# Kernel optimization log

Hardware: AMD Instinct MI355X
Metric: run time of the kernel (lower is better)

Reference implementation:

```python
import jax, jax.numpy as jnp
import numpy as np

N, G, H = 262144, 512, 16
EPS = 1e-5

Q_MAT = jnp.array([[0.0, 0.0, 1.0], [1.0, 0.0, 0.0], [0.0, 1.0, 0.0]], dtype=jnp.float32)
Q_TENSOR = jnp.kron(Q_MAT, Q_MAT)  # 9x9


def setup_inputs() -> dict:
    key = jax.random.key(0)
    ks = jax.random.split(key, 10)
    # sorted node->graph ids, every graph guaranteed non-empty
    gid = jnp.sort(jnp.concatenate([
        jnp.arange(G, dtype=jnp.int32),
        jax.random.randint(ks[0], (N - G,), 0, G, dtype=jnp.int32)]))
    return {
        'x00': jax.random.normal(ks[1], (N, 4 * H), jnp.float32),
        'x10': jax.random.normal(ks[2], (N, H, 3), jnp.float32),
        'x01': jax.random.normal(ks[3], (N, H, 3), jnp.float32),
        'x11': jax.random.normal(ks[4], (N, H, 9), jnp.float32),
        'pos': jax.random.normal(ks[5], (N, 6), jnp.float32),
        'graph_ids': gid,
        'num_graphs': G,
        'bn_gamma': jnp.ones((4 * H,), jnp.float32),
        'bn_beta': jnp.zeros((4 * H,), jnp.float32),
        'lin_w': jax.random.normal(ks[6], (3, 4 * H), jnp.float32) * 0.1,
        'lin_b': jnp.zeros((3,), jnp.float32),
        'w10': jax.random.normal(ks[7], (1, H), jnp.float32) * 0.3,
        'w01': jax.random.normal(ks[8], (1, H), jnp.float32) * 0.3,
        'w11': jax.random.normal(ks[9], (1, H), jnp.float32) * 0.3,
    }


def _graph_norm(x, seg, num_seg, gamma, beta):
    # per-graph mean/var normalization over nodes ('gn')
    cnt = jax.ops.segment_sum(jnp.ones((x.shape[0],), x.dtype), seg, num_segments=num_seg)
    cnt = jnp.maximum(cnt, 1.0)[:, None]
    mean = jax.ops.segment_sum(x, seg, num_segments=num_seg) / cnt
    var = jax.ops.segment_sum(x * x, seg, num_segments=num_seg) / cnt - mean * mean
    xn = (x - mean[seg]) * jax.lax.rsqrt(var[seg] + EPS)
    return xn * gamma + beta


def _segment_softmax(logits, seg, num_seg):
    m = jax.ops.segment_max(logits, seg, num_segments=num_seg)
    e = jnp.exp(logits - m[seg])
    s = jax.ops.segment_sum(e, seg, num_segments=num_seg)
    return e / s[seg]


def _project_r(r_vector):
    # SVD projection to nearest rotation (sign-corrected)
    norm = jnp.clip(jnp.linalg.norm(r_vector, axis=1, keepdims=True), 1e-5, None)
    r_vector = r_vector / jax.lax.stop_gradient(norm)  # norm is detached in torch
    # einops 'b (d c) -> b c d' with c=3
    r_ = jnp.transpose(r_vector.reshape(-1, 3, 3), (0, 2, 1))
    U, S, Vh = jnp.linalg.svd(r_, full_matrices=False)
    rot_pos = U @ Vh
    Vh_neg = Vh.at[:, 2, :].multiply(-1.0)
    rot_neg = U @ Vh_neg
    det = jnp.linalg.det(rot_pos)
    return jnp.where(det[:, None, None] > 0, rot_pos, rot_neg)


def reference(x00, x10, x01, x11, pos, graph_ids, num_graphs,
              bn_gamma, bn_beta, lin_w, lin_b, w10, w01, w11):
    seg = graph_ids
    Gn = num_graphs
    # BN('gn') + Linear -> 3 per-node logits
    xn = _graph_norm(x00, seg, Gn, bn_gamma, bn_beta)
    logits = xn @ lin_w.T + lin_b                       # [N,3]
    W = _segment_softmax(logits, seg, Gn)                # per-graph softmax over nodes
    w0, w1, w2 = W[:, 0:1], W[:, 1:2], W[:, 2:3]
    # weighted per-graph sums (dgl.sum_nodes)
    ab = jnp.concatenate([x10, x01], axis=-1)            # [N,H,6]
    mean_ab = jax.ops.segment_sum(ab * w1[:, :, None], seg, num_segments=Gn)   # [G,H,6]
    r_sum = jax.ops.segment_sum(x11 * w0[:, :, None], seg, num_segments=Gn)    # [G,H,9]
    m1m2 = jax.ops.segment_sum(pos * w2, seg, num_segments=Gn)                 # [G,6]
    m1, m2 = m1m2[:, 0:3], m1m2[:, 3:]
    # GLinear head: channel-mixing H -> 1 per degree type (no bias)
    out10 = jnp.einsum('oc,gcd->god', w10, mean_ab[:, :, :3])[:, 0, :]  # [G,3]
    out01 = jnp.einsum('oc,gcd->god', w01, mean_ab[:, :, 3:6])[:, 0, :]
    out11 = jnp.einsum('oc,gcd->god', w11, r_sum)[:, 0, :]              # [G,9]
    # permutation back to input frame
    r_vector = jnp.einsum('ij,gj->gi', Q_TENSOR, out11)
    trans_b = jnp.einsum('ij,gj->gi', Q_MAT, out01)
    trans_a = jnp.einsum('ij,gj->gi', Q_MAT, out10)
    rot_mat = _project_r(r_vector)
    t = m2 + trans_b - (rot_mat @ m1[..., None])[..., 0] - (rot_mat @ trans_a[..., None])[..., 0]
    return rot_mat, t, r_vector
```

## Files before the change

### kernel.cpp

```cpp
#include <hip/hip_runtime.h>
#include <cstdint>
#include <cstddef>

#define GG 512
#define NF 64
#define EPSF 1e-5f

__device__ __forceinline__ void atomAddF(float* p, float v) {
    unsafeAtomicAdd(p, v);
}

__global__ __launch_bounds__(256) void k_stats(const float* __restrict__ x00, const int* __restrict__ gid,
                        float* __restrict__ gsum, float* __restrict__ gsq,
                        float* __restrict__ gcnt, int N)
{
    int w = (blockIdx.x * blockDim.x + threadIdx.x) >> 6;
    int lane = threadIdx.x & 63;
    long base = (long)w * 64;
    int gf = gid[base];
    int gl = gid[base + 63];
    if (gf == gl) {
        const float4* p = reinterpret_cast<const float4*>(x00 + base * NF) + lane;
        float s0=0,s1=0,s2=0,s3=0,q0=0,q1=0,q2=0,q3=0;
        #pragma unroll
        for (int k = 0; k < 16; ++k) {
            float4 v = p[k * 64];
            s0+=v.x; s1+=v.y; s2+=v.z; s3+=v.w;
            q0=fmaf(v.x,v.x,q0); q1=fmaf(v.y,v.y,q1); q2=fmaf(v.z,v.z,q2); q3=fmaf(v.w,v.w,q3);
        }
        #pragma unroll
        for (int m = 16; m < 64; m <<= 1) {
            s0+=__shfl_xor(s0,m); s1+=__shfl_xor(s1,m); s2+=__shfl_xor(s2,m); s3+=__shfl_xor(s3,m);
            q0+=__shfl_xor(q0,m); q1+=__shfl_xor(q1,m); q2+=__shfl_xor(q2,m); q3+=__shfl_xor(q3,m);
        }
        if (lane < 16) {
            float* ds = gsum + gf * NF + lane * 4;
            float* dq = gsq  + gf * NF + lane * 4;
            atomAddF(ds+0,s0); atomAddF(ds+1,s1); atomAddF(ds+2,s2); atomAddF(ds+3,s3);
            atomAddF(dq+0,q0); atomAddF(dq+1,q1); atomAddF(dq+2,q2); atomAddF(dq+3,q3);
        }
        if (lane == 0) atomAddF(&gcnt[gf], 64.0f);
    } else {
        int myg = gid[base + lane];
        int cur = gf;
        float s = 0.f, q = 0.f, cnt = 0.f;
        for (int k = 0; k < 64; ++k) {
            int g = __shfl(myg, k);
            if (g != cur) {
                atomAddF(&gsum[cur * NF + lane], s);
                atomAddF(&gsq [cur * NF + lane], q);
                if (lane == 0) atomAddF(&gcnt[cur], cnt);
                s = q = cnt = 0.f; cur = g;
            }
            float v = x00[(base + k) * NF + lane];
            s += v; q = fmaf(v, v, q); cnt += 1.f;
        }
        atomAddF(&gsum[cur * NF + lane], s);
        atomAddF(&gsq [cur * NF + lane], q);
        if (lane == 0) atomAddF(&gcnt[cur], cnt);
    }
}

__global__ void k_prep(const float* __restrict__ gsum, const float* __restrict__ gsq,
                       const float* __restrict__ gcnt,
                       const float* __restrict__ gamma, const float* __restrict__ beta,
                       const float* __restrict__ lin_w, const float* __restrict__ lin_b,
                       float* __restrict__ Aeff, float* __restrict__ Beff)
{
    int g = blockIdx.x;
    int c = threadIdx.x;
    float cnt = fmaxf(gcnt[g], 1.f);
    float mean = gsum[g * NF + c] / cnt;
    float var  = gsq [g * NF + c] / cnt - mean * mean;
    float rs = rsqrtf(var + EPSF);
    float ga = gamma[c], be = beta[c];
    #pragma unroll
    for (int j = 0; j < 3; ++j) {
        float wv = lin_w[j * NF + c];
        Aeff[((long)g * 3 + j) * NF + c] = rs * ga * wv;
        float term = (be - mean * rs * ga) * wv;
        #pragma unroll
        for (int m = 32; m; m >>= 1) term += __shfl_xor(term, m);
        if (c == 0) Beff[g * 3 + j] = term + lin_b[j];
    }
}

__global__ __launch_bounds__(128) void k_logits(const float* __restrict__ x00, const int* __restrict__ gid,
                         const float* __restrict__ pos,
                         const float* __restrict__ Aeff, const float* __restrict__ Beff,
                         float* __restrict__ ebp, float* __restrict__ accum, int N)
{
    __shared__ float T2[2][64 * 68];
    int wid = threadIdx.x >> 6;
    int lane = threadIdx.x & 63;
    long chunk = (long)blockIdx.x * 2 + wid;
    long base = chunk * 64;
    float* T = T2[wid];

    const float* src = x00 + base * NF;
    #pragma unroll
    for (int k = 0; k < 16; ++k) {
        int fl = k * 256 + lane * 4;
        float4 v = *reinterpret_cast<const float4*>(src + fl);
        int n = fl >> 6, c = fl & 63;
        *reinterpret_cast<float4*>(&T[n * 68 + c]) = v;
    }
    __syncthreads();

    int gf = gid[base], gl = gid[base + 63];
    float l0, l1, l2;
    int g_l;
    if (gf == gl) {
        g_l = gf;
        const float* ap = Aeff + (size_t)gf * 192;
        float a0a=0,a0b=0,a1a=0,a1b=0,a2a=0,a2b=0;
        #pragma unroll
        for (int t = 0; t < 16; ++t) {
            float4 xv = *reinterpret_cast<const float4*>(&T[lane * 68 + 4 * t]);
            float4 w0 = *reinterpret_cast<const float4*>(ap + 4 * t);
            float4 w1 = *reinterpret_cast<const float4*>(ap + 64 + 4 * t);
            float4 w2 = *reinterpret_cast<const float4*>(ap + 128 + 4 * t);
            a0a = fmaf(xv.x,w0.x,fmaf(xv.y,w0.y,a0a)); a0b = fmaf(xv.z,w0.z,fmaf(xv.w,w0.w,a0b));
            a1a = fmaf(xv.x,w1.x,fmaf(xv.y,w1.y,a1a)); a1b = fmaf(xv.z,w1.z,fmaf(xv.w,w1.w,a1b));
            a2a = fmaf(xv.x,w2.x,fmaf(xv.y,w2.y,a2a)); a2b = fmaf(xv.z,w2.z,fmaf(xv.w,w2.w,a2b));
        }
        l0 = a0a + a0b + Beff[gf*3+0];
        l1 = a1a + a1b + Beff[gf*3+1];
        l2 = a2a + a2b + Beff[gf*3+2];
    } else {
        g_l = gid[base + lane];
        const float* ap = Aeff + (size_t)g_l * 192;
        float a0=0,a1=0,a2=0;
        #pragma unroll
        for (int t = 0; t < 16; ++t) {
            float4 xv = *reinterpret_cast<const float4*>(&T[lane * 68 + 4 * t]);
            float4 w0 = *reinterpret_cast<const float4*>(ap + 4 * t);
            float4 w1 = *reinterpret_cast<const float4*>(ap + 64 + 4 * t);
            float4 w2 = *reinterpret_cast<const float4*>(ap + 128 + 4 * t);
            a0 = fmaf(xv.x,w0.x,fmaf(xv.y,w0.y,fmaf(xv.z,w0.z,fmaf(xv.w,w0.w,a0))));
            a1 = fmaf(xv.x,w1.x,fmaf(xv.y,w1.y,fmaf(xv.z,w1.z,fmaf(xv.w,w1.w,a1))));
            a2 = fmaf(xv.x,w2.x,fmaf(xv.y,w2.y,fmaf(xv.z,w2.z,fmaf(xv.w,w2.w,a2))));
        }
        l0 = a0 + Beff[g_l*3+0];
        l1 = a1 + Beff[g_l*3+1];
        l2 = a2 + Beff[g_l*3+2];
    }
    float e0 = expf(l0), e1 = expf(l1), e2 = expf(l2);
    long node = base + lane;
    ebp[node]            = e0;
    ebp[(long)N + node]  = e1;
    ebp[2L * N + node]   = e2;

    const float* pp = pos + node * 6;
    float2 v01 = *reinterpret_cast<const float2*>(pp);
    float2 v23 = *reinterpret_cast<const float2*>(pp + 2);
    float2 v45 = *reinterpret_cast<const float2*>(pp + 4);
    float p0 = v01.x*e2, p1 = v01.y*e2, p2 = v23.x*e2, p3 = v23.y*e2, p4 = v45.x*e2, p5 = v45.y*e2;
    if (gf == gl) {
        #pragma unroll
        for (int m = 1; m < 64; m <<= 1) {
            e0+=__shfl_xor(e0,m); e1+=__shfl_xor(e1,m); e2+=__shfl_xor(e2,m);
            p0+=__shfl_xor(p0,m); p1+=__shfl_xor(p1,m); p2+=__shfl_xor(p2,m);
            p3+=__shfl_xor(p3,m); p4+=__shfl_xor(p4,m); p5+=__shfl_xor(p5,m);
        }
        if (lane == 0) {
            float* dst = accum + (long)gf * 32;
            atomAddF(dst+16,p0); atomAddF(dst+17,p1); atomAddF(dst+18,p2);
            atomAddF(dst+19,p3); atomAddF(dst+20,p4); atomAddF(dst+21,p5);
            atomAddF(dst+22,e0); atomAddF(dst+23,e1); atomAddF(dst+24,e2);
        }
    } else {
        float* dst = accum + (long)g_l * 32;
        atomAddF(dst+16,p0); atomAddF(dst+17,p1); atomAddF(dst+18,p2);
        atomAddF(dst+19,p3); atomAddF(dst+20,p4); atomAddF(dst+21,p5);
        atomAddF(dst+22,e0); atomAddF(dst+23,e1); atomAddF(dst+24,e2);
    }
}

__global__ __launch_bounds__(256) void k_w11(const float* __restrict__ x11,
        const float* __restrict__ ebp, const int* __restrict__ gid,
        const float* __restrict__ w11, float* __restrict__ accum, int N)
{
    __shared__ float LD[64 * 148];
    __shared__ float EE[64];
    int tid = threadIdx.x;
    long tb = (long)blockIdx.x * 64;

    const float4* src = reinterpret_cast<const float4*>(x11 + tb * 144);
    float4 v[9];
    #pragma unroll
    for (int u = 0; u < 9; ++u) v[u] = src[tid + 256 * u];
    if (tid < 64) EE[tid] = ebp[tb + tid];

    #pragma unroll
    for (int u = 0; u < 9; ++u) {
        int fi = 4 * (tid + 256 * u);
        int n = fi / 144, k = fi % 144;
        *reinterpret_cast<float4*>(&LD[n * 148 + k]) = v[u];
    }
    __syncthreads();

    float w[16];
    #pragma unroll
    for (int c = 0; c < 16; ++c) w[c] = w11[c];

    float y[3]; int nn[3], dd[3];
    #pragma unroll
    for (int r = 0; r < 3; ++r) {
        int idx = tid + 256 * r;
        nn[r] = idx / 9; dd[r] = idx - 9 * nn[r];
        y[r] = 0.f;
        if (r < 2 || tid < 64) {
            float s = 0.f;
            #pragma unroll
            for (int c = 0; c < 16; ++c)
                s = fmaf(w[c], LD[nn[r] * 148 + c * 9 + dd[r]], s);
            y[r] = EE[nn[r]] * s;
        }
    }

    int gf = gid[tb], gl = gid[tb + 63];
    if (gf == gl) {
        __syncthreads();
        float* F = LD;
        #pragma unroll
        for (int r = 0; r < 3; ++r)
            if (r < 2 || tid < 64) F[dd[r] * 64 + nn[r]] = y[r];
        __syncthreads();
        if (tid < 9) {
            float s = 0.f;
            #pragma unroll
            for (int n = 0; n < 64; ++n) s += F[tid * 64 + n];
            atomAddF(accum + (long)gf * 32 + 6 + tid, s);
        }
    } else {
        #pragma unroll
        for (int r = 0; r < 3; ++r)
            if (r < 2 || tid < 64)
                atomAddF(accum + (long)gid[tb + nn[r]] * 32 + 6 + dd[r], y[r]);
    }
}

__global__ __launch_bounds__(256) void k_w1001(const float* __restrict__ x10,
        const float* __restrict__ x01, const float* __restrict__ ebp,
        const int* __restrict__ gid,
        const float* __restrict__ w10, const float* __restrict__ w01,
        float* __restrict__ accum, int N)
{
    __shared__ float LDa[64 * 52];
    __shared__ float LDb[64 * 52];
    __shared__ float EE[64];
    int tid = threadIdx.x;
    long tb = (long)blockIdx.x * 64;

    const float4* sa = reinterpret_cast<const float4*>(x10 + tb * 48);
    const float4* sb = reinterpret_cast<const float4*>(x01 + tb * 48);
    float4 va[3], vb[3];
    #pragma unroll
    for (int u = 0; u < 3; ++u) { va[u] = sa[tid + 256 * u]; vb[u] = sb[tid + 256 * u]; }
    if (tid < 64) EE[tid] = ebp[(long)N + tb + tid];

    #pragma unroll
    for (int u = 0; u < 3; ++u) {
        int fi = 4 * (tid + 256 * u);
        int n = fi / 48, k = fi % 48;
        *reinterpret_cast<float4*>(&LDa[n * 52 + k]) = va[u];
        *reinterpret_cast<float4*>(&LDb[n * 52 + k]) = vb[u];
    }
    __syncthreads();

    float wA[16], wB[16];
    #pragma unroll
    for (int c = 0; c < 16; ++c) { wA[c] = w10[c]; wB[c] = w01[c]; }

    float y[2]; int nn[2], dd[2], ar[2];
    #pragma unroll
    for (int r = 0; r < 2; ++r) {
        int idx = tid + 256 * r;
        ar[r] = idx / 192;
        int j = idx - 192 * ar[r];
        nn[r] = j / 3; dd[r] = j - 3 * nn[r];
        y[r] = 0.f;
        if (r < 1 || tid < 128) {
            const float* Lx = ar[r] ? LDb : LDa;
            float s = 0.f;
            #pragma unroll
            for (int c = 0; c < 16; ++c) {
                float wc = ar[r] ? wB[c] : wA[c];
                s = fmaf(wc, Lx[nn[r] * 52 + c * 3 + dd[r]], s);
            }
            y[r] = EE[nn[r]] * s;
        }
    }

    int gf = gid[tb], gl = gid[tb + 63];
    if (gf == gl) {
        __syncthreads();
        float* F = LDa;
        #pragma unroll
        for (int r = 0; r < 2; ++r)
            if (r < 1 || tid < 128) F[ar[r] * 192 + dd[r] * 64 + nn[r]] = y[r];
        __syncthreads();
        if (tid < 6) {
            int a = tid / 3, d = tid - 3 * a;
            float s = 0.f;
            #pragma unroll
            for (int n = 0; n < 64; ++n) s += F[a * 192 + d * 64 + n];
            atomAddF(accum + (long)gf * 32 + a * 3 + d, s);
        }
    } else {
        #pragma unroll
        for (int r = 0; r < 2; ++r)
            if (r < 1 || tid < 128)
                atomAddF(accum + (long)gid[tb + nn[r]] * 32 + ar[r] * 3 + dd[r], y[r]);
    }
}

#define JROT(p, q) do { \
    float apq_ = S[p][q]; \
    if (fabsf(apq_) > 1e-20f) { \
        float app_ = S[p][p], aqq_ = S[q][q]; \
        float tau_ = (aqq_ - app_) / (2.0f * apq_); \
        float tt_ = copysignf(1.0f, tau_) / (fabsf(tau_) + sqrtf(1.0f + tau_ * tau_)); \
        float cc_ = 1.0f / sqrtf(1.0f + tt_ * tt_); \
        float ssn_ = tt_ * cc_; \
        _Pragma("unroll") for (int kk = 0; kk < 3; ++kk) { \
            float skp = S[kk][p], skq = S[kk][q]; \
            S[kk][p] = cc_ * skp - ssn_ * skq; S[kk][q] = ssn_ * skp + cc_ * skq; } \
        _Pragma("unroll") for (int kk = 0; kk < 3; ++kk) { \
            float spk = S[p][kk], sqk = S[q][kk]; \
            S[p][kk] = cc_ * spk - ssn_ * sqk; S[q][kk] = ssn_ * spk + cc_ * sqk; } \
        _Pragma("unroll") for (int kk = 0; kk < 3; ++kk) { \
            float vkp = V[kk][p], vkq = V[kk][q]; \
            V[kk][p] = cc_ * vkp - ssn_ * vkq; V[kk][q] = ssn_ * vkp + cc_ * vkq; } \
    } \
} while (0)

__global__ void k_final(const float* __restrict__ accum, float* __restrict__ out)
{
    int g = blockIdx.x * blockDim.x + threadIdx.x;
    if (g >= GG) return;
    const float* A_ = accum + (long)g * 32;
    float i0 = 1.f / A_[22], i1 = 1.f / A_[23], i2 = 1.f / A_[24];

    float o10[3], o01[3], o11[9];
    #pragma unroll
    for (int d = 0; d < 3; ++d) { o10[d] = A_[d] * i1; o01[d] = A_[3 + d] * i1; }
    #pragma unroll
    for (int d = 0; d < 9; ++d) o11[d] = A_[6 + d] * i0;

    float m1v[3], m2v[3];
    #pragma unroll
    for (int d = 0; d < 3; ++d) { m1v[d] = A_[16 + d] * i2; m2v[d] = A_[19 + d] * i2; }

    int sig[3]; sig[0] = 2; sig[1] = 0; sig[2] = 1;
    float rv[9];
    #pragma unroll
    for (int a = 0; a < 3; ++a)
        #pragma unroll
        for (int b = 0; b < 3; ++b)
            rv[a * 3 + b] = o11[sig[a] * 3 + sig[b]];
    float ta[3], tb[3];
    #pragma unroll
    for (int a = 0; a < 3; ++a) { ta[a] = o10[sig[a]]; tb[a] = o01[sig[a]]; }

    float nn = 0.f;
    #pragma unroll
    for (int k = 0; k < 9; ++k) nn += rv[k] * rv[k];
    float invn = 1.f / fmaxf(sqrtf(nn), 1e-5f);
    float M[3][3];
    #pragma unroll
    for (int a = 0; a < 3; ++a)
        #pragma unroll
        for (int b = 0; b < 3; ++b)
            M[a][b] = rv[b * 3 + a] * invn;

    float S[3][3], V[3][3];
    #pragma unroll
    for (int a = 0; a < 3; ++a)
        #pragma unroll
        for (int b = 0; b < 3; ++b) {
            float acc = 0.f;
            #pragma unroll
            for (int k = 0; k < 3; ++k) acc += M[k][a] * M[k][b];
            S[a][b] = acc;
            V[a][b] = (a == b) ? 1.f : 0.f;
        }
    for (int sw = 0; sw < 12; ++sw) { JROT(0, 1); JROT(0, 2); JROT(1, 2); }

    float l0 = S[0][0], l1 = S[1][1], l2 = S[2][2];
    float e0x = V[0][0], e0y = V[1][0], e0z = V[2][0];
    float e1x = V[0][1], e1y = V[1][1], e1z = V[2][1];
    float e2x = V[0][2], e2y = V[1][2], e2z = V[2][2];
    float tfl;
    if (l0 < l1) { tfl=l0;l0=l1;l1=tfl; tfl=e0x;e0x=e1x;e1x=tfl; tfl=e0y;e0y=e1y;e1y=tfl; tfl=e0z;e0z=e1z;e1z=tfl; }
    if (l0 < l2) { tfl=l0;l0=l2;l2=tfl; tfl=e0x;e0x=e2x;e2x=tfl; tfl=e0y;e0y=e2y;e2y=tfl; tfl=e0z;e0z=e2z;e2z=tfl; }
    if (l1 < l2) { tfl=l1;l1=l2;l2=tfl; tfl=e1x;e1x=e2x;e2x=tfl; tfl=e1y;e1y=e2y;e2y=tfl; tfl=e1z;e1z=e2z;e2z=tfl; }

    float c2x = e0y * e1z - e0z * e1y;
    float c2y = e0z * e1x - e0x * e1z;
    float c2z = e0x * e1y - e0y * e1x;
    float cn = rsqrtf(fmaxf(c2x * c2x + c2y * c2y + c2z * c2z, 1e-30f));
    c2x *= cn; c2y *= cn; c2z *= cn;

    float u0x = M[0][0] * e0x + M[0][1] * e0y + M[0][2] * e0z;
    float u0y = M[1][0] * e0x + M[1][1] * e0y + M[1][2] * e0z;
    float u0z = M[2][0] * e0x + M[2][1] * e0y + M[2][2] * e0z;
    float un = rsqrtf(fmaxf(u0x * u0x + u0y * u0y + u0z * u0z, 1e-30f));
    u0x *= un; u0y *= un; u0z *= un;
    float u1x = M[0][0] * e1x + M[0][1] * e1y + M[0][2] * e1z;
    float u1y = M[1][0] * e1x + M[1][1] * e1y + M[1][2] * e1z;
    float u1z = M[2][0] * e1x + M[2][1] * e1y + M[2][2] * e1z;
    float dp = u0x * u1x + u0y * u1y + u0z * u1z;
    u1x -= dp * u0x; u1y -= dp * u0y; u1z -= dp * u0z;
    un = rsqrtf(fmaxf(u1x * u1x + u1y * u1y + u1z * u1z, 1e-30f));
    u1x *= un; u1y *= un; u1z *= un;
    float u2x = u0y * u1z - u0z * u1y;
    float u2y = u0z * u1x - u0x * u1z;
    float u2z = u0x * u1y - u0y * u1x;

    float R[3][3];
    R[0][0] = u0x * e0x + u1x * e1x + u2x * c2x;
    R[0][1] = u0x * e0y + u1x * e1y + u2x * c2y;
    R[0][2] = u0x * e0z + u1x * e1z + u2x * c2z;
    R[1][0] = u0y * e0x + u1y * e1x + u2y * c2x;
    R[1][1] = u0y * e0y + u1y * e1y + u2y * c2y;
    R[1][2] = u0y * e0z + u1y * e1z + u2y * c2z;
    R[2][0] = u0z * e0x + u1z * e1x + u2z * c2x;
    R[2][1] = u0z * e0y + u1z * e1y + u2z * c2y;
    R[2][2] = u0z * e0z + u1z * e1z + u2z * c2z;

    float tv[3];
    #pragma unroll
    for (int a = 0; a < 3; ++a) {
        float acc = m2v[a] + tb[a];
        #pragma unroll
        for (int b = 0; b < 3; ++b) acc -= R[a][b] * (m1v[b] + ta[b]);
        tv[a] = acc;
    }

    #pragma unroll
    for (int k = 0; k < 9; ++k) out[(long)g * 9 + k] = R[k / 3][k % 3];
    #pragma unroll
    for (int a = 0; a < 3; ++a) out[(long)GG * 9 + (long)g * 3 + a] = tv[a];
    #pragma unroll
    for (int k = 0; k < 9; ++k) out[(long)GG * 12 + (long)g * 9 + k] = rv[k];
}

extern "C" void kernel_launch(void* const* d_in, const int* in_sizes, int n_in,
                              void* d_out, int out_size, void* d_ws, size_t ws_size,
                              hipStream_t stream)
{
    const float* x00   = (const float*)d_in[0];
    const float* x10   = (const float*)d_in[1];
    const float* x01   = (const float*)d_in[2];
    const float* x11   = (const float*)d_in[3];
    const float* pos   = (const float*)d_in[4];
    const int*   gid   = (const int*)d_in[5];
    const float* gamma = (const float*)d_in[7];
    const float* beta  = (const float*)d_in[8];
    const float* lin_w = (const float*)d_in[9];
    const float* lin_b = (const float*)d_in[10];
    const float* w10   = (const float*)d_in[11];
    const float* w01   = (const float*)d_in[12];
    const float* w11   = (const float*)d_in[13];
    float* out = (float*)d_out;

    const int N = in_sizes[0] / NF;

    float* ws = (float*)d_ws;
    float* gsum  = ws;
    float* gsq   = gsum + GG * 64;
    float* gcnt  = gsq + GG * 64;
    float* accum = gcnt + GG;
    float* Aeff  = accum + GG * 32;
    float* Beff  = Aeff + GG * 192;
    float* ebp   = Beff + GG * 3;

    size_t zeroBytes = (size_t)(GG * 64 * 2 + GG + GG * 32) * sizeof(float);
    hipMemsetAsync(d_ws, 0, zeroBytes, stream);

    int blocksA = (N / 64) / 4;
    int blocksL = (N / 64) / 2;
    int blocksT = N / 64;

    k_stats <<<blocksA, 256, 0, stream>>>(x00, gid, gsum, gsq, gcnt, N);
    k_prep  <<<GG, 64, 0, stream>>>(gsum, gsq, gcnt, gamma, beta, lin_w, lin_b, Aeff, Beff);
    k_logits<<<blocksL, 128, 0, stream>>>(x00, gid, pos, Aeff, Beff, ebp, accum, N);
    k_w11   <<<blocksT, 256, 0, stream>>>(x11, ebp, gid, w11, accum, N);
    k_w1001 <<<blocksT, 256, 0, stream>>>(x10, x01, ebp, gid, w10, w01, accum, N);
    k_final <<<(GG + 63) / 64, 64, 0, stream>>>(accum, out);
}
```

Before: 180.0 us.

## Stream x11/x10/x01 reductions through registers with multi-tile blocks and prefetch

Rewrites the two weighted-reduction kernels so each block handles several tiles (256 or 512 nodes). Rows are loaded straight into registers and contracted there, which removes the full LDS staging of x11, x10 and x01. Results build up in per-graph register accumulators that are flushed only when the graph id changes, with the next tile loaded before the current one is computed. The aim is to cut LDS traffic, barriers and atomics, and to hide load latency, at the cost of fewer blocks and per-lane strided global loads that may coalesce less well.

```diff
diff --git a/kernel.cpp b/kernel.cpp
--- a/kernel.cpp
+++ b/kernel.cpp
@@ -181,64 +181,103 @@
         const float* __restrict__ ebp, const int* __restrict__ gid,
         const float* __restrict__ w11, float* __restrict__ accum, int N)
 {
-    __shared__ float LD[64 * 148];
-    __shared__ float EE[64];
-    int tid = threadIdx.x;
-    long tb = (long)blockIdx.x * 64;
-
-    const float4* src = reinterpret_cast<const float4*>(x11 + tb * 144);
-    float4 v[9];
-    #pragma unroll
-    for (int u = 0; u < 9; ++u) v[u] = src[tid + 256 * u];
-    if (tid < 64) EE[tid] = ebp[tb + tid];
-
-    #pragma unroll
-    for (int u = 0; u < 9; ++u) {
-        int fi = 4 * (tid + 256 * u);
-        int n = fi / 144, k = fi % 144;
-        *reinterpret_cast<float4*>(&LD[n * 148 + k]) = v[u];
-    }
-    __syncthreads();
-
-    float w[16];
-    #pragma unroll
-    for (int c = 0; c < 16; ++c) w[c] = w11[c];
-
-    float y[3]; int nn[3], dd[3];
-    #pragma unroll
-    for (int r = 0; r < 3; ++r) {
-        int idx = tid + 256 * r;
-        nn[r] = idx / 9; dd[r] = idx - 9 * nn[r];
-        y[r] = 0.f;
-        if (r < 2 || tid < 64) {
-            float s = 0.f;
-            #pragma unroll
-            for (int c = 0; c < 16; ++c)
-                s = fmaf(w[c], LD[nn[r] * 148 + c * 9 + dd[r]], s);
-            y[r] = EE[nn[r]] * s;
-        }
-    }
-
-    int gf = gid[tb], gl = gid[tb + 63];
-    if (gf == gl) {
-        __syncthreads();
-        float* F = LD;
-        #pragma unroll
-        for (int r = 0; r < 3; ++r)
-            if (r < 2 || tid < 64) F[dd[r] * 64 + nn[r]] = y[r];
-        __syncthreads();
-        if (tid < 9) {
-            float s = 0.f;
-            #pragma unroll
-            for (int n = 0; n < 64; ++n) s += F[tid * 64 + n];
-            atomAddF(accum + (long)gf * 32 + 6 + tid, s);
-        }
-    } else {
-        #pragma unroll
-        for (int r = 0; r < 3; ++r)
-            if (r < 2 || tid < 64)
-                atomAddF(accum + (long)gid[tb + nn[r]] * 32 + 6 + dd[r], y[r]);
-    }
+    __shared__ float F[576];
+    const int tid = threadIdx.x;
+    const int row = tid >> 2, q = tid & 3;
+    const long blkBase = (long)blockIdx.x * 256;
+
+    float wq[4];
+    #pragma unroll
+    for (int c = 0; c < 4; ++c) wq[c] = w11[4 * q + c];
+
+    float acc[9];
+    #pragma unroll
+    for (int d = 0; d < 9; ++d) acc[d] = 0.f;
+    int cur = gid[blkBase];
+    bool dirty = false;
+
+    auto flush = [&]() {
+        if (dirty) {
+            float t0[9];
+            #pragma unroll
+            for (int d = 0; d < 9; ++d) {
+                float v = acc[d];
+                v += __shfl_xor(v, 1);
+                v += __shfl_xor(v, 2);
+                t0[d] = v;
+            }
+            if (q == 0) {
+                #pragma unroll
+                for (int d = 0; d < 9; ++d) F[row * 9 + d] = t0[d];
+            }
+            __syncthreads();
+            if (tid < 9) {
+                float s = 0.f;
+                for (int m = 0; m < 64; ++m) s += F[m * 9 + tid];
+                atomAddF(accum + (long)cur * 32 + 6 + tid, s);
+            }
+            __syncthreads();
+            #pragma unroll
+            for (int d = 0; d < 9; ++d) acc[d] = 0.f;
+            dirty = false;
+        }
+    };
+
+    auto loadT = [&](float4 (&B)[9], float& ev, int T) {
+        const float4* s = reinterpret_cast<const float4*>(x11 + (blkBase + (long)T * 64) * 144);
+        #pragma unroll
+        for (int j = 0; j < 9; ++j) B[j] = s[(size_t)row * 36 + q * 9 + j];
+        ev = ebp[blkBase + (long)T * 64 + row];
+    };
+
+    auto compT = [&](float4 (&B)[9], float ev, int T) {
+        long tb = blkBase + (long)T * 64;
+        int gf = gid[tb], gl = gid[tb + 63];
+        float z[9];
+        #pragma unroll
+        for (int d = 0; d < 9; ++d) z[d] = 0.f;
+        #pragma unroll
+        for (int j = 0; j < 9; ++j) {
+            const int i0 = 4 * j;
+            z[(i0 + 0) % 9] = fmaf(wq[(i0 + 0) / 9], B[j].x, z[(i0 + 0) % 9]);
+            z[(i0 + 1) % 9] = fmaf(wq[(i0 + 1) / 9], B[j].y, z[(i0 + 1) % 9]);
+            z[(i0 + 2) % 9] = fmaf(wq[(i0 + 2) / 9], B[j].z, z[(i0 + 2) % 9]);
+            z[(i0 + 3) % 9] = fmaf(wq[(i0 + 3) / 9], B[j].w, z[(i0 + 3) % 9]);
+        }
+        if (gf == gl) {
+            if (gf != cur) { flush(); cur = gf; }
+            #pragma unroll
+            for (int d = 0; d < 9; ++d) acc[d] = fmaf(ev, z[d], acc[d]);
+            dirty = true;
+        } else {
+            flush();
+            int gm = gid[tb + row];
+            #pragma unroll
+            for (int d = 0; d < 9; ++d) {
+                float v = z[d] * ev;
+                v += __shfl_xor(v, 1);
+                v += __shfl_xor(v, 2);
+                z[d] = v;
+            }
+            float v1 = (q == 0) ? z[0] : (q == 1) ? z[1] : (q == 2) ? z[2] : z[3];
+            float v2 = (q == 0) ? z[4] : (q == 1) ? z[5] : (q == 2) ? z[6] : z[7];
+            float* dst = accum + (long)gm * 32 + 6;
+            atomAddF(dst + q, v1);
+            atomAddF(dst + 4 + q, v2);
+            if (q == 0) atomAddF(dst + 8, z[8]);
+            cur = gl;
+        }
+    };
+
+    float4 P[9], Q[9];
+    float eP, eQ;
+    loadT(P, eP, 0);
+    loadT(Q, eQ, 1);
+    compT(P, eP, 0); loadT(P, eP, 2);
+    compT(Q, eQ, 1); loadT(Q, eQ, 3);
+    compT(P, eP, 2);
+    compT(Q, eQ, 3);
+    flush();
 }
 
 __global__ __launch_bounds__(256) void k_w1001(const float* __restrict__ x10,
@@ -247,73 +286,94 @@
         const float* __restrict__ w10, const float* __restrict__ w01,
         float* __restrict__ accum, int N)
 {
-    __shared__ float LDa[64 * 52];
-    __shared__ float LDb[64 * 52];
-    __shared__ float EE[64];
-    int tid = threadIdx.x;
-    long tb = (long)blockIdx.x * 64;
-
-    const float4* sa = reinterpret_cast<const float4*>(x10 + tb * 48);
-    const float4* sb = reinterpret_cast<const float4*>(x01 + tb * 48);
-    float4 va[3], vb[3];
-    #pragma unroll
-    for (int u = 0; u < 3; ++u) { va[u] = sa[tid + 256 * u]; vb[u] = sb[tid + 256 * u]; }
-    if (tid < 64) EE[tid] = ebp[(long)N + tb + tid];
-
-    #pragma unroll
-    for (int u = 0; u < 3; ++u) {
-        int fi = 4 * (tid + 256 * u);
-        int n = fi / 48, k = fi % 48;
-        *reinterpret_cast<float4*>(&LDa[n * 52 + k]) = va[u];
-        *reinterpret_cast<float4*>(&LDb[n * 52 + k]) = vb[u];
-    }
-    __syncthreads();
+    __shared__ float F[1632];
+    const int tid = threadIdx.x;
+    const long blkBase = (long)blockIdx.x * 512;
 
     float wA[16], wB[16];
     #pragma unroll
     for (int c = 0; c < 16; ++c) { wA[c] = w10[c]; wB[c] = w01[c]; }
 
-    float y[2]; int nn[2], dd[2], ar[2];
-    #pragma unroll
-    for (int r = 0; r < 2; ++r) {
-        int idx = tid + 256 * r;
-        ar[r] = idx / 192;
-        int j = idx - 192 * ar[r];
-        nn[r] = j / 3; dd[r] = j - 3 * nn[r];
-        y[r] = 0.f;
-        if (r < 1 || tid < 128) {
-            const float* Lx = ar[r] ? LDb : LDa;
-            float s = 0.f;
-            #pragma unroll
-            for (int c = 0; c < 16; ++c) {
-                float wc = ar[r] ? wB[c] : wA[c];
-                s = fmaf(wc, Lx[nn[r] * 52 + c * 3 + dd[r]], s);
-            }
-            y[r] = EE[nn[r]] * s;
-        }
-    }
-
-    int gf = gid[tb], gl = gid[tb + 63];
-    if (gf == gl) {
-        __syncthreads();
-        float* F = LDa;
-        #pragma unroll
-        for (int r = 0; r < 2; ++r)
-            if (r < 1 || tid < 128) F[ar[r] * 192 + dd[r] * 64 + nn[r]] = y[r];
-        __syncthreads();
-        if (tid < 6) {
-            int a = tid / 3, d = tid - 3 * a;
-            float s = 0.f;
-            #pragma unroll
-            for (int n = 0; n < 64; ++n) s += F[a * 192 + d * 64 + n];
-            atomAddF(accum + (long)gf * 32 + a * 3 + d, s);
-        }
-    } else {
-        #pragma unroll
-        for (int r = 0; r < 2; ++r)
-            if (r < 1 || tid < 128)
-                atomAddF(accum + (long)gid[tb + nn[r]] * 32 + ar[r] * 3 + dd[r], y[r]);
-    }
+    float acc10[3] = {0.f, 0.f, 0.f}, acc01[3] = {0.f, 0.f, 0.f};
+    int cur = gid[blkBase];
+    bool dirty = false;
+
+    auto flush = [&]() {
+        if (dirty) {
+            #pragma unroll
+            for (int d = 0; d < 3; ++d) {
+                F[tid * 3 + d] = acc10[d];
+                F[768 + tid * 3 + d] = acc01[d];
+            }
+            __syncthreads();
+            if (tid < 96) {
+                int arr = tid / 48;
+                int u = tid % 48, d = u % 3, seg = u / 3;
+                const float* Fs = F + arr * 768;
+                float s = 0.f;
+                #pragma unroll
+                for (int m = 0; m < 16; ++m) s += Fs[(seg * 16 + m) * 3 + d];
+                F[1536 + arr * 48 + u] = s;
+            }
+            __syncthreads();
+            if (tid < 6) {
+                int arr = tid / 3, d = tid % 3;
+                float s = 0.f;
+                #pragma unroll
+                for (int m = 0; m < 16; ++m) s += F[1536 + arr * 48 + m * 3 + d];
+                atomAddF(accum + (long)cur * 32 + arr * 3 + d, s);
+            }
+            __syncthreads();
+            #pragma unroll
+            for (int d = 0; d < 3; ++d) { acc10[d] = 0.f; acc01[d] = 0.f; }
+            dirty = false;
+        }
+    };
+
+    auto loadT = [&](float4 (&B)[12], float& ev, const float* __restrict__ arr, int T) {
+        const float4* s = reinterpret_cast<const float4*>(arr + (blkBase + (long)T * 256) * 48);
+        #pragma unroll
+        for (int j = 0; j < 12; ++j) B[j] = s[(size_t)tid * 12 + j];
+        ev = ebp[(long)N + blkBase + (long)T * 256 + tid];
+    };
+
+    auto compT = [&](float4 (&B)[12], float ev, int T, int AOFF, float (&W)[16], float (&ACC)[3]) {
+        long tb = blkBase + (long)T * 256;
+        int gf = gid[tb], gl = gid[tb + 255];
+        float z[3] = {0.f, 0.f, 0.f};
+        #pragma unroll
+        for (int j = 0; j < 12; ++j) {
+            const int i0 = 4 * j;
+            z[(i0 + 0) % 3] = fmaf(W[(i0 + 0) / 3], B[j].x, z[(i0 + 0) % 3]);
+            z[(i0 + 1) % 3] = fmaf(W[(i0 + 1) / 3], B[j].y, z[(i0 + 1) % 3]);
+            z[(i0 + 2) % 3] = fmaf(W[(i0 + 2) / 3], B[j].z, z[(i0 + 2) % 3]);
+            z[(i0 + 3) % 3] = fmaf(W[(i0 + 3) / 3], B[j].w, z[(i0 + 3) % 3]);
+        }
+        if (gf == gl) {
+            if (gf != cur) { flush(); cur = gf; }
+            #pragma unroll
+            for (int d = 0; d < 3; ++d) ACC[d] = fmaf(ev, z[d], ACC[d]);
+            dirty = true;
+        } else {
+            flush();
+            int gm = gid[tb + tid];
+            float* dst = accum + (long)gm * 32 + AOFF;
+            atomAddF(dst + 0, ev * z[0]);
+            atomAddF(dst + 1, ev * z[1]);
+            atomAddF(dst + 2, ev * z[2]);
+            cur = gl;
+        }
+    };
+
+    float4 U[12], V[12];
+    float eU, eV;
+    loadT(U, eU, x10, 0);
+    loadT(V, eV, x01, 0);
+    compT(U, eU, 0, 0, wA, acc10); loadT(U, eU, x10, 1);
+    compT(V, eV, 0, 3, wB, acc01); loadT(V, eV, x01, 1);
+    compT(U, eU, 1, 0, wA, acc10);
+    compT(V, eV, 1, 3, wB, acc01);
+    flush();
 }
 
 #define JROT(p, q) do { \
@@ -482,12 +542,13 @@
 
     int blocksA = (N / 64) / 4;
     int blocksL = (N / 64) / 2;
-    int blocksT = N / 64;
+    int blocksW11 = N / 256;
+    int blocksW10 = N / 512;
 
     k_stats <<<blocksA, 256, 0, stream>>>(x00, gid, gsum, gsq, gcnt, N);
     k_prep  <<<GG, 64, 0, stream>>>(gsum, gsq, gcnt, gamma, beta, lin_w, lin_b, Aeff, Beff);
     k_logits<<<blocksL, 128, 0, stream>>>(x00, gid, pos, Aeff, Beff, ebp, accum, N);
-    k_w11   <<<blocksT, 256, 0, stream>>>(x11, ebp, gid, w11, accum, N);
-    k_w1001 <<<blocksT, 256, 0, stream>>>(x10, x01, ebp, gid, w10, w01, accum, N);
+    k_w11   <<<blocksW11, 256, 0, stream>>>(x11, ebp, gid, w11, accum, N);
+    k_w1001 <<<blocksW10, 256, 0, stream>>>(x10, x01, ebp, gid, w10, w01, accum, N);
     k_final <<<(GG + 63) / 64, 64, 0, stream>>>(accum, out);
 }
```

Result: slower. 255.7 us (+42.0%).

## Make w11 and w10/w01 reductions persistent with double-buffered tiles

Applied to the files above, without the earlier changes.

Each block of the x11 and x10/x01 reduction kernels now handles 256 nodes as eight 32-node tiles. It prefetches the next tile into registers while computing the current one from a double-buffered LDS stage. Per-thread partial sums are carried across tiles of the same graph and flushed only when the graph changes, which cuts block count, LDS reductions and atomics. The cost is lower parallelism (4x fewer blocks), an extra barrier per tile, and some lanes idle in the 32-node tiles.

```diff
diff --git a/kernel.cpp b/kernel.cpp
--- a/kernel.cpp
+++ b/kernel.cpp
@@ -181,64 +181,94 @@
         const float* __restrict__ ebp, const int* __restrict__ gid,
         const float* __restrict__ w11, float* __restrict__ accum, int N)
 {
-    __shared__ float LD[64 * 148];
-    __shared__ float EE[64];
-    int tid = threadIdx.x;
-    long tb = (long)blockIdx.x * 64;
-
-    const float4* src = reinterpret_cast<const float4*>(x11 + tb * 144);
-    float4 v[9];
-    #pragma unroll
-    for (int u = 0; u < 9; ++u) v[u] = src[tid + 256 * u];
-    if (tid < 64) EE[tid] = ebp[tb + tid];
-
-    #pragma unroll
-    for (int u = 0; u < 9; ++u) {
-        int fi = 4 * (tid + 256 * u);
-        int n = fi / 144, k = fi % 144;
-        *reinterpret_cast<float4*>(&LD[n * 148 + k]) = v[u];
-    }
-    __syncthreads();
+    __shared__ float LD[2][32 * 148];
+    __shared__ float EE[2][32];
+    __shared__ float F[288];
+    const int tid = threadIdx.x;
+    const long blkBase = (long)blockIdx.x * 256;
+    const int T = 8;
 
     float w[16];
     #pragma unroll
     for (int c = 0; c < 16; ++c) w[c] = w11[c];
 
-    float y[3]; int nn[3], dd[3];
-    #pragma unroll
-    for (int r = 0; r < 3; ++r) {
-        int idx = tid + 256 * r;
-        nn[r] = idx / 9; dd[r] = idx - 9 * nn[r];
-        y[r] = 0.f;
-        if (r < 2 || tid < 64) {
-            float s = 0.f;
+    const int n1 = tid / 9, d1 = tid - 9 * n1;
+    const int o2 = 256 + tid;
+    const int n2s = (tid < 32) ? (o2 / 9) : 31;
+    const int d2s = (tid < 32) ? (o2 - 9 * (o2 / 9)) : 0;
+
+    float acc1 = 0.f, acc2 = 0.f;
+    int cur = gid[blkBase];
+    bool dirty = false;
+
+    auto flush = [&]() {
+        if (dirty) {
+            F[tid] = acc1;
+            if (tid < 32) F[256 + tid] = acc2;
+            __syncthreads();
+            if (tid < 9) {
+                float s = 0.f;
+                #pragma unroll
+                for (int n = 0; n < 32; ++n) s += F[n * 9 + tid];
+                atomAddF(accum + (long)cur * 32 + 6 + tid, s);
+            }
+            __syncthreads();
+            acc1 = acc2 = 0.f;
+            dirty = false;
+        }
+    };
+
+    float4 r0, r1, r2, r3, r4;
+    float eR = 0.f;
+    auto loadT = [&](int t) {
+        const float4* s = reinterpret_cast<const float4*>(x11 + (blkBase + (long)t * 32) * 144);
+        r0 = s[tid];
+        r1 = s[tid + 256];
+        r2 = s[tid + 512];
+        r3 = s[tid + 768];
+        if (tid < 128) r4 = s[tid + 1024];
+        if (tid < 32) eR = ebp[blkBase + (long)t * 32 + tid];
+    };
+    auto stageT = [&](int b) {
+        float* dst = LD[b];
+        int fi;
+        fi = 4 * tid;         *reinterpret_cast<float4*>(&dst[(fi / 144) * 148 + fi % 144]) = r0;
+        fi = 4 * (tid + 256); *reinterpret_cast<float4*>(&dst[(fi / 144) * 148 + fi % 144]) = r1;
+        fi = 4 * (tid + 512); *reinterpret_cast<float4*>(&dst[(fi / 144) * 148 + fi % 144]) = r2;
+        fi = 4 * (tid + 768); *reinterpret_cast<float4*>(&dst[(fi / 144) * 148 + fi % 144]) = r3;
+        if (tid < 128) { fi = 4 * (tid + 1024); *reinterpret_cast<float4*>(&dst[(fi / 144) * 148 + fi % 144]) = r4; }
+        if (tid < 32) EE[b][tid] = eR;
+    };
+
+    loadT(0); stageT(0); __syncthreads();
+
+    for (int t = 0; t < T; ++t) {
+        if (t + 1 < T) loadT(t + 1);
+        const float* B = LD[t & 1];
+        long tb = blkBase + (long)t * 32;
+        int gf = gid[tb], gl = gid[tb + 31];
+        float y1 = 0.f, y2 = 0.f;
+        #pragma unroll
+        for (int c = 0; c < 16; ++c) y1 = fmaf(w[c], B[n1 * 148 + c * 9 + d1], y1);
+        if (tid < 32) {
             #pragma unroll
-            for (int c = 0; c < 16; ++c)
-                s = fmaf(w[c], LD[nn[r] * 148 + c * 9 + dd[r]], s);
-            y[r] = EE[nn[r]] * s;
-        }
-    }
-
-    int gf = gid[tb], gl = gid[tb + 63];
-    if (gf == gl) {
+            for (int c = 0; c < 16; ++c) y2 = fmaf(w[c], B[n2s * 148 + c * 9 + d2s], y2);
+        }
+        if (gf == gl) {
+            if (gf != cur) { flush(); cur = gf; }
+            acc1 = fmaf(EE[t & 1][n1], y1, acc1);
+            if (tid < 32) acc2 = fmaf(EE[t & 1][n2s], y2, acc2);
+            dirty = true;
+        } else {
+            flush();
+            atomAddF(accum + (long)gid[tb + n1] * 32 + 6 + d1, EE[t & 1][n1] * y1);
+            if (tid < 32) atomAddF(accum + (long)gid[tb + n2s] * 32 + 6 + d2s, EE[t & 1][n2s] * y2);
+            cur = gl;
+        }
         __syncthreads();
-        float* F = LD;
-        #pragma unroll
-        for (int r = 0; r < 3; ++r)
-            if (r < 2 || tid < 64) F[dd[r] * 64 + nn[r]] = y[r];
-        __syncthreads();
-        if (tid < 9) {
-            float s = 0.f;
-            #pragma unroll
-            for (int n = 0; n < 64; ++n) s += F[tid * 64 + n];
-            atomAddF(accum + (long)gf * 32 + 6 + tid, s);
-        }
-    } else {
-        #pragma unroll
-        for (int r = 0; r < 3; ++r)
-            if (r < 2 || tid < 64)
-                atomAddF(accum + (long)gid[tb + nn[r]] * 32 + 6 + dd[r], y[r]);
-    }
+        if (t + 1 < T) { stageT((t + 1) & 1); __syncthreads(); }
+    }
+    flush();
 }
 
 __global__ __launch_bounds__(256) void k_w1001(const float* __restrict__ x10,
@@ -247,73 +277,93 @@
         const float* __restrict__ w10, const float* __restrict__ w01,
         float* __restrict__ accum, int N)
 {
-    __shared__ float LDa[64 * 52];
-    __shared__ float LDb[64 * 52];
-    __shared__ float EE[64];
-    int tid = threadIdx.x;
-    long tb = (long)blockIdx.x * 64;
-
-    const float4* sa = reinterpret_cast<const float4*>(x10 + tb * 48);
-    const float4* sb = reinterpret_cast<const float4*>(x01 + tb * 48);
-    float4 va[3], vb[3];
-    #pragma unroll
-    for (int u = 0; u < 3; ++u) { va[u] = sa[tid + 256 * u]; vb[u] = sb[tid + 256 * u]; }
-    if (tid < 64) EE[tid] = ebp[(long)N + tb + tid];
-
-    #pragma unroll
-    for (int u = 0; u < 3; ++u) {
-        int fi = 4 * (tid + 256 * u);
+    __shared__ float LA[2][32 * 52];
+    __shared__ float LB[2][32 * 52];
+    __shared__ float EE[2][32];
+    __shared__ float F[192];
+    const int tid = threadIdx.x;
+    const long blkBase = (long)blockIdx.x * 256;
+    const int T = 8;
+
+    const bool act = tid < 192;
+    const int arr = (tid < 96) ? 0 : 1;
+    const int rem = tid - 96 * arr;
+    const int nn = (act ? rem : 0) / 3;
+    const int dd = (act ? rem : 0) - 3 * ((act ? rem : 0) / 3);
+
+    float wsel[16];
+    #pragma unroll
+    for (int c = 0; c < 16; ++c) wsel[c] = arr ? w01[c] : w10[c];
+
+    float acc = 0.f;
+    int cur = gid[blkBase];
+    bool dirty = false;
+
+    auto flush = [&]() {
+        if (dirty) {
+            if (act) F[tid] = acc;
+            __syncthreads();
+            if (tid < 6) {
+                int a = tid / 3, d = tid - 3 * a;
+                float s = 0.f;
+                #pragma unroll
+                for (int n = 0; n < 32; ++n) s += F[a * 96 + n * 3 + d];
+                atomAddF(accum + (long)cur * 32 + a * 3 + d, s);
+            }
+            __syncthreads();
+            acc = 0.f;
+            dirty = false;
+        }
+    };
+
+    float4 a0, a1, b0, b1;
+    float eR = 0.f;
+    auto loadT = [&](int t) {
+        const float4* sa = reinterpret_cast<const float4*>(x10 + (blkBase + (long)t * 32) * 48);
+        const float4* sb = reinterpret_cast<const float4*>(x01 + (blkBase + (long)t * 32) * 48);
+        a0 = sa[tid]; b0 = sb[tid];
+        if (tid < 128) { a1 = sa[tid + 256]; b1 = sb[tid + 256]; }
+        if (tid < 32) eR = ebp[(long)N + blkBase + (long)t * 32 + tid];
+    };
+    auto stageT = [&](int b) {
+        int fi = 4 * tid;
         int n = fi / 48, k = fi % 48;
-        *reinterpret_cast<float4*>(&LDa[n * 52 + k]) = va[u];
-        *reinterpret_cast<float4*>(&LDb[n * 52 + k]) = vb[u];
-    }
-    __syncthreads();
-
-    float wA[16], wB[16];
-    #pragma unroll
-    for (int c = 0; c < 16; ++c) { wA[c] = w10[c]; wB[c] = w01[c]; }
-
-    float y[2]; int nn[2], dd[2], ar[2];
-    #pragma unroll
-    for (int r = 0; r < 2; ++r) {
-        int idx = tid + 256 * r;
-        ar[r] = idx / 192;
-        int j = idx - 192 * ar[r];
-        nn[r] = j / 3; dd[r] = j - 3 * nn[r];
-        y[r] = 0.f;
-        if (r < 1 || tid < 128) {
-            const float* Lx = ar[r] ? LDb : LDa;
-            float s = 0.f;
+        *reinterpret_cast<float4*>(&LA[b][n * 52 + k]) = a0;
+        *reinterpret_cast<float4*>(&LB[b][n * 52 + k]) = b0;
+        if (tid < 128) {
+            fi = 4 * (tid + 256);
+            n = fi / 48; k = fi % 48;
+            *reinterpret_cast<float4*>(&LA[b][n * 52 + k]) = a1;
+            *reinterpret_cast<float4*>(&LB[b][n * 52 + k]) = b1;
+        }
+        if (tid < 32) EE[b][tid] = eR;
+    };
+
+    loadT(0); stageT(0); __syncthreads();
+
+    for (int t = 0; t < T; ++t) {
+        if (t + 1 < T) loadT(t + 1);
+        const float* Bx = arr ? LB[t & 1] : LA[t & 1];
+        long tb = blkBase + (long)t * 32;
+        int gf = gid[tb], gl = gid[tb + 31];
+        float y = 0.f;
+        if (act) {
             #pragma unroll
-            for (int c = 0; c < 16; ++c) {
-                float wc = ar[r] ? wB[c] : wA[c];
-                s = fmaf(wc, Lx[nn[r] * 52 + c * 3 + dd[r]], s);
-            }
-            y[r] = EE[nn[r]] * s;
-        }
-    }
-
-    int gf = gid[tb], gl = gid[tb + 63];
-    if (gf == gl) {
+            for (int c = 0; c < 16; ++c) y = fmaf(wsel[c], Bx[nn * 52 + c * 3 + dd], y);
+        }
+        if (gf == gl) {
+            if (gf != cur) { flush(); cur = gf; }
+            if (act) acc = fmaf(EE[t & 1][nn], y, acc);
+            dirty = true;
+        } else {
+            flush();
+            if (act) atomAddF(accum + (long)gid[tb + nn] * 32 + arr * 3 + dd, EE[t & 1][nn] * y);
+            cur = gl;
+        }
         __syncthreads();
-        float* F = LDa;
-        #pragma unroll
-        for (int r = 0; r < 2; ++r)
-            if (r < 1 || tid < 128) F[ar[r] * 192 + dd[r] * 64 + nn[r]] = y[r];
-        __syncthreads();
-        if (tid < 6) {
-            int a = tid / 3, d = tid - 3 * a;
-            float s = 0.f;
-            #pragma unroll
-            for (int n = 0; n < 64; ++n) s += F[a * 192 + d * 64 + n];
-            atomAddF(accum + (long)gf * 32 + a * 3 + d, s);
-        }
-    } else {
-        #pragma unroll
-        for (int r = 0; r < 2; ++r)
-            if (r < 1 || tid < 128)
-                atomAddF(accum + (long)gid[tb + nn[r]] * 32 + ar[r] * 3 + dd[r], y[r]);
-    }
+        if (t + 1 < T) { stageT((t + 1) & 1); __syncthreads(); }
+    }
+    flush();
 }
 
 #define JROT(p, q) do { \
@@ -482,12 +532,12 @@
 
     int blocksA = (N / 64) / 4;
     int blocksL = (N / 64) / 2;
-    int blocksT = N / 64;
+    int blocksD = N / 256;
 
     k_stats <<<blocksA, 256, 0, stream>>>(x00, gid, gsum, gsq, gcnt, N);
     k_prep  <<<GG, 64, 0, stream>>>(gsum, gsq, gcnt, gamma, beta, lin_w, lin_b, Aeff, Beff);
     k_logits<<<blocksL, 128, 0, stream>>>(x00, gid, pos, Aeff, Beff, ebp, accum, N);
-    k_w11   <<<blocksT, 256, 0, stream>>>(x11, ebp, gid, w11, accum, N);
-    k_w1001 <<<blocksT, 256, 0, stream>>>(x10, x01, ebp, gid, w10, w01, accum, N);
+    k_w11   <<<blocksD, 256, 0, stream>>>(x11, ebp, gid, w11, accum, N);
+    k_w1001 <<<blocksD, 256, 0, stream>>>(x10, x01, ebp, gid, w10, w01, accum, N);
     k_final <<<(GG + 63) / 64, 64, 0, stream>>>(accum, out);
 }
```

Result: faster. 172.7 us (-4.1%).
